# Performance work log

Measured on AMD Instinct MI355X. Metric: run time of the kernel, lower is better.

## Reference

```python
import jax, jax.numpy as jnp
from jax import lax
import numpy as np

DT = jnp.float32
M = 1000          # quadrature points (torch.linspace steps=1000)
PI = float(np.pi)
EPS = 1e-12       # guards sqrt args against round-off (original asserts instead)


def _trapz(f, x):
    dx = x[1:] - x[:-1]
    return jnp.sum(0.5 * (f[..., 1:] + f[..., :-1]) * dx, axis=-1)


def _ygrid():
    return jnp.linspace(0.001, 0.999, M, dtype=DT)


def _extend(y, integ):
    # prepend linearly-extrapolated value at y=0, append 0 at y=1 (as in torch code)
    slope = (integ[..., 1] - integ[..., 0]) / (y[1] - y[0])
    v0 = integ[..., 0] - slope * y[0]
    yy = jnp.concatenate([jnp.zeros((1,), DT), y, jnp.ones((1,), DT)])
    zrs = jnp.zeros(integ.shape[:-1] + (1,), DT)
    ii = jnp.concatenate([v0[..., None], integ, zrs], axis=-1)
    return yy, ii


def eval_f(a, z):
    _a = jnp.concatenate([jnp.ones((1,), DT), a])  # [1, a0, a1]
    out = jnp.zeros_like(z)
    for i in range(3):
        for j in range(3):
            c = _a[i] * _a[j]
            if i + j == 4:
                out = out - 4.0 * c * z**4 * jnp.log(z)
            else:
                out = out + 4.0 * c * (z**4 - z**(i + j)) / (i + j - 4)
    return out


def eval_df(a, z):
    _a = jnp.concatenate([jnp.ones((1,), DT), a])
    out = jnp.zeros_like(z)
    for i in range(3):
        for j in range(3):
            out = out - 4.0 * _a[i] * _a[j] * z**(i + j)
    return (out + 4.0 * eval_f(a, z)) / z


def _bcoef(a, b):
    last = a.sum() - b.sum()
    return jnp.concatenate([jnp.ones((1,), DT), b, last[None]])  # length 4


def eval_b_(a, b, z):
    c = _bcoef(a, b)
    out = jnp.zeros_like(z)
    for i in range(4):
        for j in range(4):
            out = out + c[i] * c[j] * z**(i + j)
    return out


def eval_db(a, b, z):
    c = _bcoef(a, b)
    x = jnp.zeros_like(z)
    dx = jnp.zeros_like(z)
    for i in range(4):
        x = x + c[i] * z**i
    for i in range(1, 4):
        dx = dx + i * c[i] * z**(i - 1)
    return 2.0 * dx * x


def eval_g(a, b, z):
    return eval_b_(a, b, z) / ((1 - z) * (1 + z) * (1 + z**2))


def eval_dg(a, b, z):
    D = (1 - z) * (1 + z) * (1 + z**2)  # = 1 - z^4
    return eval_db(a, b, z) / D + 4.0 * z**3 * eval_b_(a, b, z) / D**2


def integrate_L(a, b, zs):
    y = _ygrid()
    zs_ = zs[..., None]
    z = zs_ * (1 - y) * (1 + y)
    sqrtg = jnp.sqrt(eval_g(a, b, z))
    f_over_fs = eval_f(a, z) / eval_f(a, zs_)
    arg = f_over_fs / ((1 - y)**4 * (1 + y)**4) - 1.0
    integ = sqrtg / jnp.sqrt(jnp.maximum(arg, EPS)) * y
    yy, ii = _extend(y, integ)
    return 4.0 * zs * _trapz(ii, yy) / PI


def integrate_dL(a, b, zs):
    y = _ygrid()
    zs_ = zs[..., None]
    z = zs_ * (1 - y) * (1 + y)
    fs = eval_f(a, zs_)
    g = eval_g(a, b, z)
    f_over_fs = eval_f(a, z) / fs
    df = eval_df(a, z)
    dfs = eval_df(a, zs_)
    dg = eval_dg(a, b, z)
    r4 = zs_**4 / z**4
    integ = r4 * f_over_fs * (zs_ * dfs / fs + 2 + z * dg / g) - zs_**4 / z**3 * df / fs - 2 - z * dg / g
    integ = integ * 2 * jnp.sqrt(jnp.maximum(1 - z / zs_, 0.0)) * jnp.sqrt(g) / jnp.maximum(r4 * f_over_fs - 1, EPS)**1.5
    yy, ii = _extend(y, integ)
    return _trapz(ii, yy) / PI


def integrate_V(a, b, logcoef, zs):
    coef = jnp.exp(logcoef)
    # connected piece
    y = _ygrid()
    zs_ = zs[..., None]
    z = zs_ * (1 - y) * (1 + y)
    f = eval_f(a, z)
    fg = f * eval_g(a, b, z)
    f_over_fs = f / eval_f(a, zs_)
    w = (1 - y)**2 * (1 + y)**2
    integ = jnp.sqrt(jnp.maximum(fg, EPS)) / w * (1.0 / jnp.sqrt(jnp.maximum(1 - w**2 / f_over_fs, EPS)) - 1.0) * y
    yy, ii = _extend(y, integ)
    Vc = coef * PI * 4.0 * _trapz(ii, yy) / zs
    # disconnected piece
    y2 = jnp.linspace(0.001, 1.0, M, dtype=DT)
    z2 = 1 - (1 - zs_) * y2
    fg2 = eval_f(a, z2) * eval_g(a, b, z2)
    integ2 = jnp.sqrt(jnp.maximum(fg2, EPS)) / z2**2
    yy2 = jnp.concatenate([jnp.zeros((1,), DT), y2])
    ii2 = jnp.concatenate([jnp.ones(integ2.shape[:-1] + (1,), DT), integ2], axis=-1)
    Vd = coef * PI * 2.0 * (1 - zs) * _trapz(ii2, yy2)
    return Vc - Vd


def _bisect(fun, lo, hi, iters=30):
    # keeps invariant fun(lo) >= 0 > fun(hi); matches the torch bisections
    def body(_, c):
        lo, hi = c
        mid = 0.5 * (lo + hi)
        pred = fun(mid) < 0
        return (jnp.where(pred, lo, mid), jnp.where(pred, mid, hi))
    lo, hi = lax.fori_loop(0, iters, body, (jnp.asarray(lo, DT), jnp.asarray(hi, DT)))
    return 0.5 * (lo + hi)


def get_L_max(a, b):
    zs = _bisect(lambda m: integrate_dL(a, b, m), 0.001, 0.999)
    return zs, integrate_L(a, b, zs)


def get_L_crit(a, b, logcoef, zs_max):
    zs = _bisect(lambda m: -integrate_V(a, b, logcoef, m), 0.001, zs_max)
    return zs, integrate_L(a, b, zs)


def find_zs_newton(a, b, L, init, steps=25):
    @jax.checkpoint
    def step(zs, _):
        Lz = integrate_L(a, b, zs)
        dL = integrate_dL(a, b, zs)
        zs = jnp.clip(zs - (Lz - L) / dL, 1e-4, 0.9995)
        return zs, None
    zs, _ = lax.scan(step, init, None, length=steps)
    return zs


def forward(Ls, a, b, logcoef):
    # bisection searches run under torch.no_grad in the original -> stop gradients
    a_ng = lax.stop_gradient(a)
    b_ng = lax.stop_gradient(b)
    lc_ng = lax.stop_gradient(logcoef)
    zs_max, L_max = get_L_max(a_ng, b_ng)
    zs_crit, L_crit = get_L_crit(a_ng, b_ng, lc_ng, zs_max)
    valid = Ls < L_crit
    L_eff = jnp.where(valid, Ls, 0.5 * L_crit)  # masked rows still solve a well-posed problem
    init = jnp.clip(L_eff / L_max * zs_max, 1e-4, 0.9995)  # interp1d through (0,0)-(L_max, zs_max)
    zs = find_zs_newton(a, b, L_eff, init)
    V = integrate_V(a, b, logcoef, zs)
    return jnp.where(valid, V, jnp.zeros_like(V))


def setup_inputs() -> dict:
    key = jax.random.key(0)
    k1, k2, k3 = jax.random.split(key, 3)
    B = 4096
    Ls = jax.random.uniform(k1, (B,), dtype=jnp.float32) * 0.2
    a = 0.05 * jax.random.normal(k2, (2,), dtype=jnp.float32)
    b = 0.05 * jax.random.normal(k3, (2,), dtype=jnp.float32)
    logcoef = jnp.zeros((), jnp.float32)
    return {"Ls": Ls, "a": a, "b": b, "logcoef": logcoef}


def reference(Ls, a, b, logcoef):
    return forward(Ls, a, b, logcoef)
```

## Files before the change

### kernel.cpp

```cpp
#include <hip/hip_runtime.h>
#include <math.h>

#define MQ 1000
#define PI_F 3.14159265358979323846f
#define EPSF 1e-12f
#define DYF  ((float)(0.998/999.0))
#define DY2F ((float)(0.999/999.0))
#define NG   2048
#define HG   (0.998f / (float)NG)

__device__ __forceinline__ float frcp(float x)  { return __builtin_amdgcn_rcpf(x); }
__device__ __forceinline__ float frsq(float x)  { return __builtin_amdgcn_rsqf(x); }
__device__ __forceinline__ float fsqrt(float x) { return __builtin_amdgcn_sqrtf(x); }


struct Co {
    float q1, q2, q3, q4, cf4;
    float e1, e2, e3, e4;
    float b0, b1, p3;
    float coef;
};

__device__ __forceinline__ Co make_co(const float* a, const float* b, const float* lc) {
    Co c;
    float a0 = a[0], a1 = a[1];
    float cf1 = -8.f * a0 / 3.f;
    float cf2 = -2.f * (2.f * a1 + a0 * a0);
    float cf3 = -8.f * a0 * a1;
    c.cf4 = -4.f * a1 * a1;
    c.q1 = -cf1; c.q2 = -cf2; c.q3 = -cf3; c.q4 = cf1 + cf2 + cf3 - 1.f;
    c.e1 = 2.f * a0;
    c.e2 = 2.f * a1 + a0 * a0;
    c.e3 = 2.f * a0 * a1;
    c.e4 = a1 * a1;
    c.b0 = b[0]; c.b1 = b[1];
    c.p3 = a0 + a1 - b[0] - b[1];
    c.coef = expf(lc[0]);
    return c;
}

struct Uni { float zs, fs, rfs, A4; };

__device__ __forceinline__ Uni make_uni(const Co& c, float zs) {
    Uni U; U.zs = zs;
    float z = zs;
    float lg = __logf(z);
    float t4 = c.q4 + c.cf4 * lg;
    float fz = 1.f + z * (c.q1 + z * (c.q2 + z * (c.q3 + z * t4)));
    float s  = 1.f + z * (c.e1 + z * (c.e2 + z * (c.e3 + z * c.e4)));
    U.fs = fz;
    U.rfs = frcp(fz);
    float dfs = 4.f * (fz - s) * frcp(z);
    U.A4 = zs * dfs * U.rfs - 2.f;
    return U;
}

__device__ __forceinline__ void point_LdL(const Co& c, const Uni& U,
                                          float y, float u,
                                          float& iL, float& iD) {
    float u2  = u * u;
    float ru2 = frcp(u2);
    float ru4 = ru2 * ru2;
    float z  = U.zs * u;
    float z2 = z * z, z4 = z2 * z2;
    float lg = __logf(z);
    float t4 = c.q4 + c.cf4 * lg;
    float fz = 1.f + z * (c.q1 + z * (c.q2 + z * (c.q3 + z * t4)));
    float s  = 1.f + z * (c.e1 + z * (c.e2 + z * (c.e3 + z * c.e4)));
    float P  = 1.f + z * (c.b0 + z * (c.b1 + z * c.p3));
    float dP = c.b0 + z * (2.f * c.b1 + z * (3.f * c.p3));
    float D  = 1.f - z4;
    float rsqD = frsq(D);
    float rcpD = rsqD * rsqD;
    float rcpP = frcp(P);
    float zdgg = 2.f * z * dP * rcpP + 4.f * z4 * rcpD;
    float F4 = fz * U.rfs * ru4;
    float S4 = s  * U.rfs * ru4;
    float den = fmaxf(F4 - 1.f, EPSF);
    float rs  = frsq(den);
    float sqg = P * rsqD;
    float t1  = sqg * rs;
    iL = t1 * y;
    float t = F4 * (U.A4 + zdgg) + 4.f * S4 - 2.f - zdgg;
    float rs2 = rs * rs;
    iD = t * (2.f * y) * (t1 * rs2);
}

__device__ __forceinline__ float point_Vc(const Co& c, const Uni& U,
                                          float y, float u) {
    float u2  = u * u;
    float u4  = u2 * u2;
    float ru2 = frcp(u2);
    float z  = U.zs * u;
    float z2 = z * z, z4 = z2 * z2;
    float lg = __logf(z);
    float t4 = c.q4 + c.cf4 * lg;
    float fz = 1.f + z * (c.q1 + z * (c.q2 + z * (c.q3 + z * t4)));
    float P  = 1.f + z * (c.b0 + z * (c.b1 + z * c.p3));
    float D  = 1.f - z4;
    float rsqD = frsq(D);
    float rcpD = rsqD * rsqD;
    float fg = fz * P * P * rcpD;
    float sqfg = fsqrt(fmaxf(fg, EPSF));
    float rfz = frcp(fz);
    float arg = fmaxf(1.f - u4 * U.fs * rfz, EPSF);
    float t = frsq(arg) - 1.f;
    return sqfg * ru2 * t * y;
}

__device__ __forceinline__ float point_Vd(const Co& c, const Uni& U, float y2) {
    float z  = 1.f - (1.f - U.zs) * y2;
    float z2 = z * z, z4 = z2 * z2;
    float lg = __logf(z);
    float t4 = c.q4 + c.cf4 * lg;
    float fz = 1.f + z * (c.q1 + z * (c.q2 + z * (c.q3 + z * t4)));
    float P  = 1.f + z * (c.b0 + z * (c.b1 + z * c.p3));
    float D  = 1.f - z4;
    float rsqD = frsq(D);
    float fg = fz * P * P * (rsqD * rsqD);
    float sq = fsqrt(fmaxf(fg, EPSF));
    float rz = frcp(z);
    return sq * rz * rz;
}

__device__ __forceinline__ float trapz_ext(float S, float i0, float i1, float iN) {
    float slope = (i1 - i0) * frcp(DYF);
    float v0 = i0 - slope * 0.001f;
    float yLast = 0.001f + 999.f * DYF;
    return DYF * (S - 0.5f * (i0 + iN))
         + 0.5f * (v0 + i0) * 0.001f
         + 0.5f * iN * (1.f - yLast);
}

__device__ __forceinline__ float trapz_d(float S, float q0, float qN) {
    return 0.5f * (1.f + q0) * 0.001f + DY2F * (S - 0.5f * (q0 + qN));
}

__global__ __launch_bounds__(128) void grid_eval_kernel(
        const float* a, const float* b, const float* lc, float* ws) {
    __shared__ float red[4];
    __shared__ float spx[8];
    int bid = blockIdx.x;
    int t = threadIdx.x, lane = t & 63, w = t >> 6;
    Co c = make_co(a, b, lc);
    int i = (bid < NG) ? bid : bid - NG;
    float zq = fmaf((float)i + 0.5f, HG, 0.001f);
    Uni U = make_uni(c, zq);

    if (bid < NG) {
        float sL = 0.f, sD = 0.f, l0 = 0.f, d0 = 0.f, l1 = 0.f, d1 = 0.f,
              lN = 0.f, dN = 0.f;
#pragma unroll
        for (int k = 0; k < 8; ++k) {
            if (k < 7 || t < 104) {
                int j = t + 128 * k;
                float y = fmaf((float)j, DYF, 0.001f);
                float u = 1.f - y * y;
                float iL, iD;
                point_LdL(c, U, y, u, iL, iD);
                sL += iL; sD += iD;
                if (k == 0) {
                    if (t == 0) { l0 = iL; d0 = iD; }
                    if (t == 1) { l1 = iL; d1 = iD; }
                }
                if (k == 7 && t == 103) { lN = iL; dN = iD; }
            }
        }
#pragma unroll
        for (int o = 32; o > 0; o >>= 1) {
            sL += __shfl_xor(sL, o, 64);
            sD += __shfl_xor(sD, o, 64);
        }
        if (lane == 0) { red[w] = sL; red[2 + w] = sD; }
        if (t == 0)   { spx[0] = l0; spx[3] = d0; }
        if (t == 1)   { spx[1] = l1; spx[4] = d1; }
        if (t == 103) { spx[2] = lN; spx[5] = dN; }
        __syncthreads();
        if (t == 0) {
            float SL = red[0] + red[1], SD = red[2] + red[3];
            float Lv  = 4.f * zq * trapz_ext(SL, spx[0], spx[1], spx[2]) / PI_F;
            float dLv = trapz_ext(SD, spx[3], spx[4], spx[5]) / PI_F;
            ws[16 + i] = dLv;
            ws[16 + 2 * NG + i] = Lv;
        }
    } else {
        float sc = 0.f, sd = 0.f, c0 = 0.f, c1v = 0.f, cN = 0.f,
              q0 = 0.f, qN = 0.f;
#pragma unroll
        for (int k = 0; k < 8; ++k) {
            if (k < 7 || t < 104) {
                int j = t + 128 * k;
                float y = fmaf((float)j, DYF, 0.001f);
                float u = 1.f - y * y;
                float vc = point_Vc(c, U, y, u);
                float y2 = fmaf((float)j, DY2F, 0.001f);
                float vd = point_Vd(c, U, y2);
                sc += vc; sd += vd;
                if (k == 0) {
                    if (t == 0) { c0 = vc; q0 = vd; }
                    if (t == 1) { c1v = vc; }
                }
                if (k == 7 && t == 103) { cN = vc; qN = vd; }
            }
        }
#pragma unroll
        for (int o = 32; o > 0; o >>= 1) {
            sc += __shfl_xor(sc, o, 64);
            sd += __shfl_xor(sd, o, 64);
        }
        if (lane == 0) { red[w] = sc; red[2 + w] = sd; }
        if (t == 0)   { spx[0] = c0; spx[3] = q0; }
        if (t == 1)   { spx[1] = c1v; }
        if (t == 103) { spx[2] = cN; spx[4] = qN; }
        __syncthreads();
        if (t == 0) {
            float Sc = red[0] + red[1], Sd = red[2] + red[3];
            float Vc = c.coef * PI_F * 4.f * trapz_ext(Sc, spx[0], spx[1], spx[2]) * frcp(zq);
            float Vd = c.coef * PI_F * 2.f * (1.f - zq) * trapz_d(Sd, spx[3], spx[4]);
            ws[16 + NG + i] = Vc - Vd;
        }
    }
}

__global__ __launch_bounds__(256) void scan_kernel(float* ws) {
    __shared__ int sdl, sv;
    const float* dLbuf = ws + 16;
    const float* Vbuf  = ws + 16 + NG;
    const float* Lbuf  = ws + 16 + 2 * NG;
    int t = threadIdx.x;
    if (t == 0) { sdl = NG; sv = NG; }
    __syncthreads();
#pragma unroll
    for (int r = 0; r < NG / 256; ++r) {
        int i = t + 256 * r;
        float dcur = dLbuf[i];
        float dprev = (i > 0) ? dLbuf[i - 1] : 1.f;
        if (dcur < 0.f && dprev >= 0.f) atomicMin(&sdl, i);
        float vcur = Vbuf[i];
        float vprev = (i > 0) ? Vbuf[i - 1] : -1.f;
        if (vcur > 0.f && vprev <= 0.f) atomicMin(&sv, i);
    }
    __syncthreads();
    if (t == 0) {
        int bound = sdl, iv = sv;
        float Lcrit;
        if (bound < 2) {
            Lcrit = -1.f;
        } else if (iv >= NG || iv >= bound) {
            Lcrit = Lbuf[bound - 1];
        } else if (iv == 0) {
            float z0 = 0.001f + 0.5f * HG;
            Lcrit = Lbuf[0] * 0.001f * frcp(z0);
        } else {
            float zhi = fmaf((float)iv + 0.5f, HG, 0.001f);
            float zlo = zhi - HG;
            float vhi = Vbuf[iv], vlo = Vbuf[iv - 1];
            float zc = zlo - vlo * (zhi - zlo) * frcp(fmaxf(vhi - vlo, 1e-30f));
            zc = fminf(fmaxf(zc, zlo), zhi);
            float tt = (zc - 0.001f) * frcp(HG) - 0.5f;
            int i0 = (int)tt;
            i0 = max(0, min(i0, bound - 2));
            float frac = fminf(fmaxf(tt - (float)i0, 0.f), 1.f);
            Lcrit = Lbuf[i0] + frac * (Lbuf[i0 + 1] - Lbuf[i0]);
        }
        ws[0] = Lcrit;
        ws[1] = (float)bound;
    }
}

__global__ __launch_bounds__(128) void elem_v_kernel(
        const float* Ls, const float* a, const float* b, const float* lc,
        const float* ws, float* out, int B) {
    __shared__ float red[4];
    __shared__ float spx[8];
    int wid = blockIdx.x;
    int t = threadIdx.x, lane = t & 63, w = t >> 6;
    if (wid >= B) return;

    float L_crit = ws[0];
    int bound = (int)ws[1];
    float Lq = Ls[wid];
    if (!(Lq < L_crit) || bound < 2) {
        if (t == 0) out[wid] = 0.f;
        return;
    }

    const float* dLbuf = ws + 16;
    const float* Lbuf  = ws + 16 + 2 * NG;
    int lo = -1, hi = bound - 1;
    while (hi > lo) {
        int mid = (lo + hi + 1) >> 1;
        if (Lbuf[mid] < Lq) lo = mid; else hi = mid - 1;
    }
    float zs;
    if (lo < 0) {
        float z0 = 0.001f + 0.5f * HG;
        zs = z0 * Lq * frcp(fmaxf(Lbuf[0], 1e-20f));
    } else {
        int seg = min(lo, bound - 2);
        float zl = fmaf((float)seg + 0.5f, HG, 0.001f);
        float Ll = Lbuf[seg],  Lh = Lbuf[seg + 1];
        float dl = dLbuf[seg] * HG, dh = dLbuf[seg + 1] * HG;
        float s = fminf(fmaxf((Lq - Ll) * frcp(fmaxf(Lh - Ll, 1e-20f)), 0.f), 1.f);
#pragma unroll
        for (int it = 0; it < 2; ++it) {
            float s2 = s * s, s3 = s2 * s;
            float H  = (2.f*s3 - 3.f*s2 + 1.f) * Ll + (s3 - 2.f*s2 + s) * dl
                     + (-2.f*s3 + 3.f*s2) * Lh + (s3 - s2) * dh;
            float Hp = (6.f*s2 - 6.f*s) * (Ll - Lh)
                     + (3.f*s2 - 4.f*s + 1.f) * dl + (3.f*s2 - 2.f*s) * dh;
            float step = (H - Lq) * frcp(Hp);
            if (fabsf(Hp) > 1e-20f) s = fminf(fmaxf(s - step, 0.f), 1.f);
        }
        zs = fmaf(s, HG, zl);
    }
    zs = fminf(fmaxf(zs, 1e-4f), 0.9995f);

    Co c = make_co(a, b, lc);
    Uni U = make_uni(c, zs);
    float sc = 0.f, sd = 0.f, c0 = 0.f, c1v = 0.f, cN = 0.f, q0 = 0.f, qN = 0.f;
#pragma unroll
    for (int k = 0; k < 8; ++k) {
        if (k < 7 || t < 104) {
            int j = t + 128 * k;
            float y = fmaf((float)j, DYF, 0.001f);
            float u = 1.f - y * y;
            float vc = point_Vc(c, U, y, u);
            float y2 = fmaf((float)j, DY2F, 0.001f);
            float vd = point_Vd(c, U, y2);
            sc += vc; sd += vd;
            if (k == 0) {
                if (t == 0) { c0 = vc; q0 = vd; }
                if (t == 1) { c1v = vc; }
            }
            if (k == 7 && t == 103) { cN = vc; qN = vd; }
        }
    }
#pragma unroll
    for (int o = 32; o > 0; o >>= 1) {
        sc += __shfl_xor(sc, o, 64);
        sd += __shfl_xor(sd, o, 64);
    }
    if (lane == 0) { red[w] = sc; red[2 + w] = sd; }
    if (t == 0)   { spx[0] = c0; spx[3] = q0; }
    if (t == 1)   { spx[1] = c1v; }
    if (t == 103) { spx[2] = cN; spx[4] = qN; }
    __syncthreads();
    if (t == 0) {
        float Sc = red[0] + red[1], Sd = red[2] + red[3];
        float Vc = c.coef * PI_F * 4.f * trapz_ext(Sc, spx[0], spx[1], spx[2]) * frcp(zs);
        float Vd = c.coef * PI_F * 2.f * (1.f - zs) * trapz_d(Sd, spx[3], spx[4]);
        out[wid] = Vc - Vd;
    }
}

extern "C" void kernel_launch(void* const* d_in, const int* in_sizes, int n_in,
                              void* d_out, int out_size, void* d_ws, size_t ws_size,
                              hipStream_t stream) {
    const float* Ls = (const float*)d_in[0];
    const float* a  = (const float*)d_in[1];
    const float* b  = (const float*)d_in[2];
    const float* lc = (const float*)d_in[3];
    float* out = (float*)d_out;
    float* ws  = (float*)d_ws;
    int B = in_sizes[0];

    grid_eval_kernel<<<2 * NG, 128, 0, stream>>>(a, b, lc, ws);
    scan_kernel<<<1, 256, 0, stream>>>(ws);
    elem_v_kernel<<<B, 128, 0, stream>>>(Ls, a, b, lc, ws, out, B);
}
```

Before: 94.64 us.

## Interpolate V from precomputed grid and fuse scan into per-element kernel

```diff
diff --git a/kernel.cpp b/kernel.cpp
--- a/kernel.cpp
+++ b/kernel.cpp
@@ -8,6 +8,7 @@
 #define DY2F ((float)(0.999/999.0))
 #define NG   2048
 #define HG   (0.998f / (float)NG)
+#define ZT   0.02f
 
 __device__ __forceinline__ float frcp(float x)  { return __builtin_amdgcn_rcpf(x); }
 __device__ __forceinline__ float frsq(float x)  { return __builtin_amdgcn_rsqf(x); }
@@ -136,6 +137,34 @@
     return 0.5f * (1.f + q0) * 0.001f + DY2F * (S - 0.5f * (q0 + qN));
 }
 
+__device__ __forceinline__ float wave_V(const Co& c, const Uni& U, int lane) {
+    float sc = 0.f, sd = 0.f, c0 = 0.f, cN = 0.f, q0 = 0.f, qN = 0.f;
+#pragma unroll
+    for (int k = 0; k < 16; ++k) {
+        if (k < 15 || lane < 40) {
+            int j = lane + 64 * k;
+            float y = fmaf((float)j, DYF, 0.001f);
+            float u = 1.f - y * y;
+            float vc = point_Vc(c, U, y, u);
+            float y2 = fmaf((float)j, DY2F, 0.001f);
+            float vd = point_Vd(c, U, y2);
+            sc += vc; sd += vd;
+            if (k == 0)  { c0 = vc; q0 = vd; }
+            if (k == 15) { cN = vc; qN = vd; }
+        }
+    }
+#pragma unroll
+    for (int o = 32; o > 0; o >>= 1) {
+        sc += __shfl_xor(sc, o, 64);
+        sd += __shfl_xor(sd, o, 64);
+    }
+    float i0 = __shfl(c0, 0, 64), i1 = __shfl(c0, 1, 64), iN = __shfl(cN, 39, 64);
+    float p0 = __shfl(q0, 0, 64), pN = __shfl(qN, 39, 64);
+    float Vc = c.coef * PI_F * 4.f * trapz_ext(sc, i0, i1, iN) * frcp(U.zs);
+    float Vd = c.coef * PI_F * 2.f * (1.f - U.zs) * trapz_d(sd, p0, pN);
+    return Vc - Vd;
+}
+
 __global__ __launch_bounds__(128) void grid_eval_kernel(
         const float* a, const float* b, const float* lc, float* ws) {
     __shared__ float red[4];
@@ -222,17 +251,23 @@
     }
 }
 
-__global__ __launch_bounds__(256) void scan_kernel(float* ws) {
-    __shared__ int sdl, sv;
+__global__ __launch_bounds__(64) void elem_out_kernel(
+        const float* Ls, const float* a, const float* b, const float* lc,
+        const float* ws, float* out, int B) {
+    __shared__ int sdl, sv, nlist;
+    __shared__ float sLcrit;
+    __shared__ int lidx[64];
+    __shared__ float lzs[64];
     const float* dLbuf = ws + 16;
     const float* Vbuf  = ws + 16 + NG;
     const float* Lbuf  = ws + 16 + 2 * NG;
     int t = threadIdx.x;
-    if (t == 0) { sdl = NG; sv = NG; }
+
+    if (t == 0) { sdl = NG; sv = NG; nlist = 0; }
     __syncthreads();
 #pragma unroll
-    for (int r = 0; r < NG / 256; ++r) {
-        int i = t + 256 * r;
+    for (int r = 0; r < NG / 64; ++r) {
+        int i = t + 64 * r;
         float dcur = dLbuf[i];
         float dprev = (i > 0) ? dLbuf[i - 1] : 1.f;
         if (dcur < 0.f && dprev >= 0.f) atomicMin(&sdl, i);
@@ -241,8 +276,9 @@
         if (vcur > 0.f && vprev <= 0.f) atomicMin(&sv, i);
     }
     __syncthreads();
+    int bound = sdl;
+    int iv = sv;
     if (t == 0) {
-        int bound = sdl, iv = sv;
         float Lcrit;
         if (bound < 2) {
             Lcrit = -1.f;
@@ -263,94 +299,75 @@
             float frac = fminf(fmaxf(tt - (float)i0, 0.f), 1.f);
             Lcrit = Lbuf[i0] + frac * (Lbuf[i0 + 1] - Lbuf[i0]);
         }
-        ws[0] = Lcrit;
-        ws[1] = (float)bound;
-    }
-}
-
-__global__ __launch_bounds__(128) void elem_v_kernel(
-        const float* Ls, const float* a, const float* b, const float* lc,
-        const float* ws, float* out, int B) {
-    __shared__ float red[4];
-    __shared__ float spx[8];
-    int wid = blockIdx.x;
-    int t = threadIdx.x, lane = t & 63, w = t >> 6;
-    if (wid >= B) return;
-
-    float L_crit = ws[0];
-    int bound = (int)ws[1];
-    float Lq = Ls[wid];
-    if (!(Lq < L_crit) || bound < 2) {
-        if (t == 0) out[wid] = 0.f;
-        return;
-    }
-
-    const float* dLbuf = ws + 16;
-    const float* Lbuf  = ws + 16 + 2 * NG;
-    int lo = -1, hi = bound - 1;
-    while (hi > lo) {
-        int mid = (lo + hi + 1) >> 1;
-        if (Lbuf[mid] < Lq) lo = mid; else hi = mid - 1;
-    }
-    float zs;
-    if (lo < 0) {
-        float z0 = 0.001f + 0.5f * HG;
-        zs = z0 * Lq * frcp(fmaxf(Lbuf[0], 1e-20f));
-    } else {
-        int seg = min(lo, bound - 2);
-        float zl = fmaf((float)seg + 0.5f, HG, 0.001f);
-        float Ll = Lbuf[seg],  Lh = Lbuf[seg + 1];
-        float dl = dLbuf[seg] * HG, dh = dLbuf[seg + 1] * HG;
-        float s = fminf(fmaxf((Lq - Ll) * frcp(fmaxf(Lh - Ll, 1e-20f)), 0.f), 1.f);
-#pragma unroll
-        for (int it = 0; it < 2; ++it) {
-            float s2 = s * s, s3 = s2 * s;
-            float H  = (2.f*s3 - 3.f*s2 + 1.f) * Ll + (s3 - 2.f*s2 + s) * dl
-                     + (-2.f*s3 + 3.f*s2) * Lh + (s3 - s2) * dh;
-            float Hp = (6.f*s2 - 6.f*s) * (Ll - Lh)
-                     + (3.f*s2 - 4.f*s + 1.f) * dl + (3.f*s2 - 2.f*s) * dh;
-            float step = (H - Lq) * frcp(Hp);
-            if (fabsf(Hp) > 1e-20f) s = fminf(fmaxf(s - step, 0.f), 1.f);
-        }
-        zs = fmaf(s, HG, zl);
-    }
-    zs = fminf(fmaxf(zs, 1e-4f), 0.9995f);
-
-    Co c = make_co(a, b, lc);
-    Uni U = make_uni(c, zs);
-    float sc = 0.f, sd = 0.f, c0 = 0.f, c1v = 0.f, cN = 0.f, q0 = 0.f, qN = 0.f;
-#pragma unroll
-    for (int k = 0; k < 8; ++k) {
-        if (k < 7 || t < 104) {
-            int j = t + 128 * k;
-            float y = fmaf((float)j, DYF, 0.001f);
-            float u = 1.f - y * y;
-            float vc = point_Vc(c, U, y, u);
-            float y2 = fmaf((float)j, DY2F, 0.001f);
-            float vd = point_Vd(c, U, y2);
-            sc += vc; sd += vd;
-            if (k == 0) {
-                if (t == 0) { c0 = vc; q0 = vd; }
-                if (t == 1) { c1v = vc; }
-            }
-            if (k == 7 && t == 103) { cN = vc; qN = vd; }
-        }
-    }
-#pragma unroll
-    for (int o = 32; o > 0; o >>= 1) {
-        sc += __shfl_xor(sc, o, 64);
-        sd += __shfl_xor(sd, o, 64);
-    }
-    if (lane == 0) { red[w] = sc; red[2 + w] = sd; }
-    if (t == 0)   { spx[0] = c0; spx[3] = q0; }
-    if (t == 1)   { spx[1] = c1v; }
-    if (t == 103) { spx[2] = cN; spx[4] = qN; }
+        sLcrit = Lcrit;
+    }
     __syncthreads();
-    if (t == 0) {
-        float Sc = red[0] + red[1], Sd = red[2] + red[3];
-        float Vc = c.coef * PI_F * 4.f * trapz_ext(Sc, spx[0], spx[1], spx[2]) * frcp(zs);
-        float Vd = c.coef * PI_F * 2.f * (1.f - zs) * trapz_d(Sd, spx[3], spx[4]);
-        out[wid] = Vc - Vd;
+    float L_crit = sLcrit;
+
+    int e = blockIdx.x * 64 + t;
+    if (e < B) {
+        float Lq = Ls[e];
+        if (!(Lq < L_crit) || bound < 2) {
+            out[e] = 0.f;
+        } else {
+            int lo = -1, hi = bound - 1;
+            while (hi > lo) {
+                int mid = (lo + hi + 1) >> 1;
+                if (Lbuf[mid] < Lq) lo = mid; else hi = mid - 1;
+            }
+            float zs;
+            if (lo < 0) {
+                float z0 = 0.001f + 0.5f * HG;
+                zs = z0 * Lq * frcp(fmaxf(Lbuf[0], 1e-20f));
+            } else {
+                int seg = min(lo, bound - 2);
+                float zl = fmaf((float)seg + 0.5f, HG, 0.001f);
+                float Ll = Lbuf[seg],  Lh = Lbuf[seg + 1];
+                float dl = dLbuf[seg] * HG, dh = dLbuf[seg + 1] * HG;
+                float s = fminf(fmaxf((Lq - Ll) * frcp(fmaxf(Lh - Ll, 1e-20f)), 0.f), 1.f);
+#pragma unroll
+                for (int it = 0; it < 2; ++it) {
+                    float s2 = s * s, s3 = s2 * s;
+                    float H  = (2.f*s3 - 3.f*s2 + 1.f) * Ll + (s3 - 2.f*s2 + s) * dl
+                             + (-2.f*s3 + 3.f*s2) * Lh + (s3 - s2) * dh;
+                    float Hp = (6.f*s2 - 6.f*s) * (Ll - Lh)
+                             + (3.f*s2 - 4.f*s + 1.f) * dl + (3.f*s2 - 2.f*s) * dh;
+                    float step = (H - Lq) * frcp(Hp);
+                    if (fabsf(Hp) > 1e-20f) s = fminf(fmaxf(s - step, 0.f), 1.f);
+                }
+                zs = fmaf(s, HG, zl);
+            }
+            zs = fminf(fmaxf(zs, 1e-4f), 0.9995f);
+
+            if (zs >= ZT) {
+                float tt = (zs - 0.001f) * frcp(HG) - 0.5f;
+                int i0 = (int)tt;
+                i0 = max(1, min(i0, NG - 3));
+                float s = tt - (float)i0;
+                float vm = Vbuf[i0 - 1], v0 = Vbuf[i0], v1 = Vbuf[i0 + 1], v2 = Vbuf[i0 + 2];
+                float wm = -s * (s - 1.f) * (s - 2.f) * (1.f / 6.f);
+                float w0 = (s + 1.f) * (s - 1.f) * (s - 2.f) * 0.5f;
+                float w1 = -(s + 1.f) * s * (s - 2.f) * 0.5f;
+                float w2 = (s + 1.f) * s * (s - 1.f) * (1.f / 6.f);
+                out[e] = wm * vm + w0 * v0 + w1 * v1 + w2 * v2;
+            } else {
+                int slot = atomicAdd(&nlist, 1);
+                lidx[slot] = e;
+                lzs[slot] = zs;
+            }
+        }
+    }
+    __syncthreads();
+
+    int n = nlist;
+    if (n > 0) {
+        Co c = make_co(a, b, lc);
+        for (int q = 0; q < n; ++q) {
+            float zq = lzs[q];
+            Uni U = make_uni(c, zq);
+            float V = wave_V(c, U, t);
+            if (t == 0) out[lidx[q]] = V;
+        }
     }
 }
 
@@ -366,6 +383,6 @@
     int B = in_sizes[0];
 
     grid_eval_kernel<<<2 * NG, 128, 0, stream>>>(a, b, lc, ws);
-    scan_kernel<<<1, 256, 0, stream>>>(ws);
-    elem_v_kernel<<<B, 128, 0, stream>>>(Ls, a, b, lc, ws, out, B);
-}
+    int blocksB = (B + 63) / 64;
+    elem_out_kernel<<<blocksB, 64, 0, stream>>>(Ls, a, b, lc, ws, out, B);
+}
```

After: 107.9 us. 14.0% more time.
